# Performance work log

Measured on AMD Instinct MI355X. Metric: run time of the kernel, lower is better.

The kernel has to match this reference:

```python
import jax, jax.numpy as jnp
import numpy as np
import math

NUM_FREQS = 16  # module init num_freqs


def posenc(x, nf):
    # x [..., D] -> [..., D*2*nf]
    freqs = 2.0 ** jnp.arange(nf, dtype=x.dtype)
    xf = x[..., None] * freqs  # [..., D, nf]
    enc = jnp.concatenate([jnp.sin(xf), jnp.cos(xf)], axis=-1)  # [..., D, 2nf]
    return enc.reshape(x.shape[:-1] + (x.shape[-1] * 2 * nf,))


def plucker(rays):
    # rays [..., 6] = [origin, direction] -> [d_norm, cross(o, d_norm)]
    o, dv = rays[..., :3], rays[..., 3:]
    dn = dv / (jnp.linalg.norm(dv, axis=-1, keepdims=True) + 1e-8)
    return jnp.concatenate([dn, jnp.cross(o, dn)], axis=-1)


def grid_sample_bilinear(img, grid):
    # img [N,C,H,W], grid [N,Hg,Wg,2] in [-1,1], align_corners=True, zeros padding
    N, C, H, W = img.shape
    x = (grid[..., 0] + 1.0) * 0.5 * (W - 1)
    y = (grid[..., 1] + 1.0) * 0.5 * (H - 1)
    x0 = jnp.floor(x); x1 = x0 + 1.0
    y0 = jnp.floor(y); y1 = y0 + 1.0
    wx1 = x - x0; wx0 = 1.0 - wx1
    wy1 = y - y0; wy0 = 1.0 - wy1

    def gather(ix, iy):
        valid = ((ix >= 0) & (ix <= W - 1) & (iy >= 0) & (iy <= H - 1)).astype(img.dtype)
        ixc = jnp.clip(ix, 0, W - 1).astype(jnp.int32)
        iyc = jnp.clip(iy, 0, H - 1).astype(jnp.int32)
        vals = jax.vmap(lambda im, iyn, ixn: im[:, iyn, ixn])(img, iyc, ixc)  # [N,C,Hg,Wg]
        return vals * valid[:, None]

    return (gather(x0, y0) * (wx0 * wy0)[:, None]
            + gather(x1, y0) * (wx1 * wy0)[:, None]
            + gather(x0, y1) * (wx0 * wy1)[:, None]
            + gather(x1, y1) * (wx1 * wy1)[:, None])


def _forward(xref, mask_ref, ray_points, rays, R, T, focal, W1, b1, W2, b2, Wv, bv, Wd):
    F = NUM_FREQS
    b, n, hw, c = xref.shape
    d = ray_points.shape[3]
    res = int(math.sqrt(hw))
    # mask (already at res x res; nearest resize is identity)
    xref = xref * mask_ref.reshape(b, n, hw, 1)
    # project sample points into all n+1 camera NDC frames
    pts = ray_points[:, 0]  # [b,hw,d,3]
    p_view = jnp.einsum('bhdk,bvkj->bvhdj', pts, R) + T[:, :, None, None]  # [b,n+1,hw,d,3]
    ndc = focal[:, :, None, None, None] * p_view[..., :2] / p_view[..., 2:3]
    grid = jax.lax.stop_gradient(jnp.clip(jnp.nan_to_num(-ndc[:, 1:]), -1.2, 1.2))
    grid = grid.reshape(b * n, hw, d, 2)
    img = xref.reshape(b * n, res, res, c).transpose(0, 3, 1, 2)  # [(bn),c,res,res]
    pf = grid_sample_bilinear(img, grid)  # [(bn),c,hw,d]
    plane_features = pf.reshape(b, n, c, hw, d).transpose(0, 1, 3, 4, 2)  # [b,n,hw,d,c]

    xyz_iv = p_view                       # view-space points [b,n+1,hw,d,3]
    xyz_iv_enc = posenc(xyz_iv, F)        # [b,n+1,hw,d,6F]

    # target rays (view 0) expressed in every view frame
    o_t, d_t = rays[:, 0, :, :3], rays[:, 0, :, 3:]
    o_iv = jnp.einsum('bhk,bvkj->bvhj', o_t, R) + T[:, :, None]
    d_iv = jnp.einsum('bhk,bvkj->bvhj', d_t, R)
    cam_iv = jnp.concatenate([o_iv, d_iv], -1)[:, 1:]  # [b,n,hw,6]
    cam_iv = jnp.broadcast_to(cam_iv[:, :, :, None, :], (b, n, hw, d, 6))
    cam_iv_enc = posenc(plucker(cam_iv), F // 2)  # [b,n,hw,d,6F]

    xyz_grid = jnp.broadcast_to(xyz_iv_enc[:, :1], (b, n, hw, d, xyz_iv_enc.shape[-1]))
    # reference-view ray origins in target frame
    o_r = rays[:, 1:, :, :3]
    o_tg = jnp.einsum('bnhk,bkj->bnhj', o_r, R[:, 0]) + T[:, 0][:, None, None]
    cam_feat = jnp.broadcast_to(o_tg[:, :, :, None, :], (b, n, hw, d, 3))
    cam_feat_enc = posenc(cam_feat, F)

    plane_in = jnp.concatenate([plane_features, xyz_iv_enc[:, 1:], xyz_iv[:, 1:],
                                cam_iv_enc, cam_iv[..., 3:]], axis=-1)  # [b,n,hw,d,326]
    h = jax.nn.silu(plane_in @ W1 + b1)
    pf_final = h @ W2 + b2  # [b,n,hw,d,C]

    attn_in = jnp.concatenate([plane_features, xyz_grid,
                               jnp.broadcast_to(xyz_iv[:, :1], (b, n, hw, d, 3)),
                               cam_feat, cam_feat_enc], axis=-1)  # [b,n,hw,d,326]
    attn = jax.nn.softmax(attn_in @ Wv + bv, axis=1)  # softmax over views
    fused = (pf_final * attn).sum(1)  # [b,hw,d,C]
    out = fused @ Wd  # decoder (no bias) -> [b,hw,d,1]
    return jnp.concatenate([fused, out], axis=-1), attn


def setup_inputs() -> dict:
    B, N, RES, D, C = 1, 4, 32, 32, 128
    HW = RES * RES
    IN_DIM = C + NUM_FREQS * 3 * 4 + 6  # 326
    key = jax.random.key(0)
    ks = jax.random.split(key, 16)
    xref = jax.random.normal(ks[0], (B, N, HW, C), jnp.float32)
    mask_ref = (jax.random.uniform(ks[1], (B, N, RES, RES)) > 0.1).astype(jnp.float32)
    ray_points = jax.random.uniform(ks[2], (B, 1, HW, D, 3), minval=-0.5, maxval=0.5)
    o = jax.random.uniform(ks[3], (B, N + 1, HW, 3), minval=-0.2, maxval=0.2)
    dirs = jax.random.normal(ks[4], (B, N + 1, HW, 3))
    dirs = dirs / jnp.linalg.norm(dirs, axis=-1, keepdims=True)
    rays = jnp.concatenate([o, dirs], -1)
    R = jnp.linalg.qr(jax.random.normal(ks[5], (B, N + 1, 3, 3)))[0]
    T = jnp.concatenate([jax.random.uniform(ks[6], (B, N + 1, 2), minval=-0.2, maxval=0.2),
                         jax.random.uniform(ks[7], (B, N + 1, 1), minval=2.0, maxval=2.5)], -1)
    focal = jax.random.uniform(ks[8], (B, N + 1), minval=0.8, maxval=1.2)
    W1 = jax.random.normal(ks[9], (IN_DIM, C)) / np.sqrt(IN_DIM)
    b1 = jnp.zeros((C,), jnp.float32)
    W2 = jax.random.normal(ks[10], (C, C)) / np.sqrt(C)
    b2 = jnp.zeros((C,), jnp.float32)
    Wv = jax.random.normal(ks[11], (IN_DIM, 1)) / np.sqrt(IN_DIM)
    bv = jnp.zeros((1,), jnp.float32)
    Wd = jax.random.normal(ks[12], (C, 1)) * 0.01  # zero_module in source; small random for meaningful baseline
    return {"xref": xref, "mask_ref": mask_ref, "ray_points": ray_points, "rays": rays,
            "R": R, "T": T, "focal": focal, "W1": W1, "b1": b1, "W2": W2, "b2": b2,
            "Wv": Wv, "bv": bv, "Wd": Wd}


def reference(xref, mask_ref, ray_points, rays, R, T, focal, W1, b1, W2, b2, Wv, bv, Wd):
    return _forward(xref, mask_ref, ray_points, rays, R, T, focal, W1, b1, W2, b2, Wv, bv, Wd)
```

## Files before the change

kernel.cpp:

```cpp
#include <hip/hip_runtime.h>
#include <hip/hip_bf16.h>
#include <math.h>

#define XH 1024
#define XD 32
#define XC 128
#define XK 326

typedef __attribute__((ext_vector_type(8))) short bf16x8;
typedef __attribute__((ext_vector_type(4))) float f32x4;

__device__ __forceinline__ unsigned short f2b(float f) {
  unsigned u = __float_as_uint(f);
  return (unsigned short)((u + 0x7FFFu + ((u >> 16) & 1u)) >> 16);
}
__device__ __forceinline__ float b2f(unsigned short b) {
  return __uint_as_float(((unsigned)b) << 16);
}
__device__ __forceinline__ unsigned pk2bf(float v0, float v1) {
  __hip_bfloat162 h = __float22bfloat162_rn(make_float2(v0, v1));
  return *reinterpret_cast<unsigned*>(&h);
}

#define WT1 (12 * 8 * 64)
#define WT2 (4 * 8 * 64)

__global__ void prep_frags(const float* __restrict__ W1,
                           const float* __restrict__ W2,
                           unsigned int* __restrict__ ws) {
  int f = blockIdx.x * 256 + threadIdx.x;
  if (f >= WT1 + WT2) return;
  const float* W; int KMAX; int fl; size_t hoff, loff;
  if (f < WT1) { W = W1; KMAX = XK; fl = f; hoff = 0; loff = WT1; }
  else { W = W2; KMAX = XC; fl = f - WT1; hoff = 2 * (size_t)WT1; loff = 2 * (size_t)WT1 + WT2; }
  int l = fl & 63, ct = (fl >> 6) & 7, kc = fl >> 9;
  int c = ct * 16 + (l & 15);
  int kbase = kc * 32 + 8 * (l >> 4);
  unsigned hi[4], lo[4];
  #pragma unroll
  for (int jj = 0; jj < 4; ++jj) {
    int k0 = kbase + 2 * jj;
    float w0 = (k0     < KMAX) ? W[k0 * XC + c]       : 0.f;
    float w1 = (k0 + 1 < KMAX) ? W[(k0 + 1) * XC + c] : 0.f;
    unsigned short h0 = f2b(w0); unsigned short l0 = f2b(w0 - b2f(h0));
    unsigned short h1 = f2b(w1); unsigned short l1 = f2b(w1 - b2f(h1));
    hi[jj] = (unsigned)h0 | ((unsigned)h1 << 16);
    lo[jj] = (unsigned)l0 | ((unsigned)l1 << 16);
  }
  uint4 vh; vh.x = hi[0]; vh.y = hi[1]; vh.z = hi[2]; vh.w = hi[3];
  uint4 vl; vl.x = lo[0]; vl.y = lo[1]; vl.z = lo[2]; vl.w = lo[3];
  *(uint4*)(ws + (hoff + fl) * 4) = vh;
  *(uint4*)(ws + (loff + fl) * 4) = vl;
}


__global__ __launch_bounds__(512, 4)
void nerf_main(const float* __restrict__ xref,
               const float* __restrict__ mask,
               const float* __restrict__ rpts,
               const float* __restrict__ rays,
               const float* __restrict__ Rm,
               const float* __restrict__ Tm,
               const float* __restrict__ focp,
               const float* __restrict__ b1p,
               const float* __restrict__ b2p,
               const float* __restrict__ Wvp,
               const float* __restrict__ bvp,
               const float* __restrict__ Wdp,
               const bf16x8* __restrict__ wfrag,
               float* __restrict__ out0,
               float* __restrict__ out1)
{
  const int h = blockIdx.x;
  const int tid = threadIdx.x;

  __shared__ float sFoc[5];
  __shared__ float sRay[5][6];
  __shared__ float sOiv[5][3];
  __shared__ float sDiv[5][3];
  __shared__ float sPlk[4][6];
  __shared__ float sOtg[4][3];
  __shared__ float sPv[5][32][3];
  __shared__ float sBc[4][32][4];
  __shared__ int   sBp[4][32][4];
  __shared__ float sWv[XK];
  __shared__ float sAt[32];
  __shared__ float sBt[4];
  __shared__ float sLogit[4][32];
  __shared__ float sAw[4][32];
  __shared__ float sOutPart[4][32];
  __shared__ __align__(16) unsigned short sEnc2[4][128];
  __shared__ __align__(16) unsigned char uMem[65536];
  unsigned short* sFcHi = (unsigned short*)uMem;
  unsigned short* sFcLo = (unsigned short*)(uMem + 32768);
  unsigned short* sHbHi = (unsigned short*)(uMem + 32768);
  unsigned short* sHbLo = sHbHi + 32 * 128;
  float*          sOut  = (float*)uMem;

  for (int i = tid; i < 5;  i += 512) sFoc[i] = focp[i];
  for (int i = tid; i < 30; i += 512) { int v = i / 6, j = i % 6; sRay[v][j] = rays[(v*XH + h)*6 + j]; }
  for (int i = tid; i < XK; i += 512) sWv[i] = Wvp[i];

  if (tid < 160) {
    int v = tid >> 5, d = tid & 31;
    float p0 = rpts[(h*XD + d)*3 + 0];
    float p1 = rpts[(h*XD + d)*3 + 1];
    float p2 = rpts[(h*XD + d)*3 + 2];
    #pragma unroll
    for (int j = 0; j < 3; ++j)
      sPv[v][d][j] = p0*Rm[v*9 + j] + p1*Rm[v*9 + 3 + j] + p2*Rm[v*9 + 6 + j] + Tm[v*3 + j];
  } else if (tid < 165) {
    int v = tid - 160;
    float r0 = rays[(0*XH + h)*6 + 0], r1 = rays[(0*XH + h)*6 + 1], r2 = rays[(0*XH + h)*6 + 2];
    float r3 = rays[(0*XH + h)*6 + 3], r4 = rays[(0*XH + h)*6 + 4], r5 = rays[(0*XH + h)*6 + 5];
    #pragma unroll
    for (int j = 0; j < 3; ++j) {
      sOiv[v][j] = r0*Rm[v*9 + j] + r1*Rm[v*9 + 3 + j] + r2*Rm[v*9 + 6 + j] + Tm[v*3 + j];
      sDiv[v][j] = r3*Rm[v*9 + j] + r4*Rm[v*9 + 3 + j] + r5*Rm[v*9 + 6 + j];
    }
  }
  if (tid >= 256) {
    int t = tid - 256;
    int d = t >> 3, sub = t & 7;
    float p0 = rpts[(h*XD + d)*3 + 0];
    float p1 = rpts[(h*XD + d)*3 + 1];
    float p2 = rpts[(h*XD + d)*3 + 2];
    float pv0[3];
    #pragma unroll
    for (int j = 0; j < 3; ++j)
      pv0[j] = p0*Rm[j] + p1*Rm[3 + j] + p2*Rm[6 + j] + Tm[j];
    float p = 0.f;
    for (int kk = sub * 12; kk < sub * 12 + 12; ++kk) {
      int comp = kk >> 5, idx = kk & 31;
      float ang = pv0[comp] * (float)(1 << (idx & 15));
      float ev = (idx < 16) ? __sinf(ang) : __cosf(ang);
      p += ev * Wvp[128 + kk];
    }
    if (sub == 0)
      for (int j = 0; j < 3; ++j) p += pv0[j] * Wvp[224 + j];
    #pragma unroll
    for (int o = 1; o < 8; o <<= 1) p += __shfl_xor(p, o);
    if (sub == 0) sAt[d] = p;
  }
  __syncthreads();

  if (tid < 4) {
    int n = tid;
    float d0 = sDiv[n+1][0], d1 = sDiv[n+1][1], d2 = sDiv[n+1][2];
    float inv = 1.f / (sqrtf(d0*d0 + d1*d1 + d2*d2) + 1e-8f);
    float n0 = d0*inv, n1 = d1*inv, n2 = d2*inv;
    float o0 = sOiv[n+1][0], o1 = sOiv[n+1][1], o2 = sOiv[n+1][2];
    sPlk[n][0] = n0; sPlk[n][1] = n1; sPlk[n][2] = n2;
    sPlk[n][3] = o1*n2 - o2*n1;
    sPlk[n][4] = o2*n0 - o0*n2;
    sPlk[n][5] = o0*n1 - o1*n0;
    #pragma unroll
    for (int j = 0; j < 3; ++j)
      sOtg[n][j] = sRay[1+n][0]*Rm[j] + sRay[1+n][1]*Rm[3 + j] + sRay[1+n][2]*Rm[6 + j] + Tm[j];
  }
  if (tid >= 32 && tid < 160) {
    int idx = tid - 32, n = idx >> 5, d = idx & 31, v = n + 1;
    float px = sPv[v][d][0], py = sPv[v][d][1], pz = sPv[v][d][2], fo = sFoc[v];
    float gx = -(fo*px)/pz, gy = -(fo*py)/pz;
    if (isnan(gx)) gx = 0.f;
    if (isnan(gy)) gy = 0.f;
    gx = fminf(fmaxf(gx, -1.2f), 1.2f);
    gy = fminf(fmaxf(gy, -1.2f), 1.2f);
    float x = (gx + 1.f)*15.5f, y = (gy + 1.f)*15.5f;
    float x0f = floorf(x), y0f = floorf(y);
    float wx1 = x - x0f, wx0 = 1.f - wx1;
    float wy1 = y - y0f, wy0 = 1.f - wy1;
    int x0i = (int)x0f, y0i = (int)y0f;
    bool vx0 = (x0f >=  0.f) & (x0f <= 31.f);
    bool vx1 = (x0f >= -1.f) & (x0f <= 30.f);
    bool vy0 = (y0f >=  0.f) & (y0f <= 31.f);
    bool vy1 = (y0f >= -1.f) & (y0f <= 30.f);
    int x0c = min(max(x0i, 0), 31), x1c = min(max(x0i + 1, 0), 31);
    int y0c = min(max(y0i, 0), 31), y1c = min(max(y0i + 1, 0), 31);
    int p00 = y0c*32 + x0c, p10 = y0c*32 + x1c, p01 = y1c*32 + x0c, p11 = y1c*32 + x1c;
    sBc[n][d][0] = wx0*wy0*((vx0 && vy0) ? mask[n*XH + p00] : 0.f);
    sBc[n][d][1] = wx1*wy0*((vx1 && vy0) ? mask[n*XH + p10] : 0.f);
    sBc[n][d][2] = wx0*wy1*((vx0 && vy1) ? mask[n*XH + p01] : 0.f);
    sBc[n][d][3] = wx1*wy1*((vx1 && vy1) ? mask[n*XH + p11] : 0.f);
    sBp[n][d][0] = p00; sBp[n][d][1] = p10; sBp[n][d][2] = p01; sBp[n][d][3] = p11;
  }
  __syncthreads();

  const int brow = tid >> 2;
  const int bn = brow & 3, bd = brow >> 2;
  const int kloc0 = (tid & 3) * 16;
  float plog = 0.f;

  {
    const float* bc = sBc[bn][bd];
    const int*   bp = sBp[bn][bd];
    const float* xb = xref + bn * XH * XC;

    float4 pf[8];
    #pragma unroll
    for (int qq = 0; qq < 2; ++qq) {
      pf[qq*4+0] = *(const float4*)(xb + bp[0] * XC + kloc0 + 4 * qq);
      pf[qq*4+1] = *(const float4*)(xb + bp[1] * XC + kloc0 + 4 * qq);
      pf[qq*4+2] = *(const float4*)(xb + bp[2] * XC + kloc0 + 4 * qq);
      pf[qq*4+3] = *(const float4*)(xb + bp[3] * XC + kloc0 + 4 * qq);
    }

    {
      int n = tid >> 7, off = tid & 127;
      float val = 0.f;
      if (off >= 3 && off < 99) {
        int kk = off - 3;
        int comp = kk >> 4, idx = kk & 15;
        float ang = sPlk[n][comp] * (float)(1 << (idx & 7));
        val = (idx < 8) ? __sinf(ang) : __cosf(ang);
      } else if (off >= 99 && off < 102) {
        val = sDiv[n + 1][off - 99];
      }
      sEnc2[n][off] = f2b(val);
    }
    if (tid >= 256 && tid < 288) {
      int t = tid - 256, n = t >> 3, sub = t & 7;
      float p = 0.f;
      for (int kk = sub * 12; kk < sub * 12 + 12; ++kk) {
        int comp = kk >> 5, idx = kk & 31;
        float ang = sOtg[n][comp] * (float)(1 << (idx & 15));
        float ev = (idx < 16) ? __sinf(ang) : __cosf(ang);
        p += ev * sWv[230 + kk];
      }
      if (sub == 0) {
        for (int j = 0; j < 3; ++j) p += sOtg[n][j] * sWv[227 + j];
        p += bvp[0];
      }
      #pragma unroll
      for (int o = 1; o < 8; o <<= 1) p += __shfl_xor(p, o);
      if (sub == 0) sBt[n] = p;
    }

    {
      int kg = kloc0;
      float vv[16];
      #pragma unroll
      for (int qq = 0; qq < 4; ++qq) {
        float4 a0, a1, a2, a3;
        if (qq < 2) {
          a0 = pf[qq*4+0]; a1 = pf[qq*4+1]; a2 = pf[qq*4+2]; a3 = pf[qq*4+3];
        } else {
          a0 = *(const float4*)(xb + bp[0] * XC + kg + 4 * qq);
          a1 = *(const float4*)(xb + bp[1] * XC + kg + 4 * qq);
          a2 = *(const float4*)(xb + bp[2] * XC + kg + 4 * qq);
          a3 = *(const float4*)(xb + bp[3] * XC + kg + 4 * qq);
        }
        #pragma unroll
        for (int j = 0; j < 4; ++j)
          vv[4 * qq + j] = bc[0]*(&a0.x)[j] + bc[1]*(&a1.x)[j]
                         + bc[2]*(&a2.x)[j] + bc[3]*(&a3.x)[j];
      }
      #pragma unroll
      for (int j = 0; j < 16; ++j) plog += vv[j] * sWv[kg + j];
      #pragma unroll
      for (int qq = 0; qq < 2; ++qq) {
        unsigned ph[4], pl[4];
        #pragma unroll
        for (int j = 0; j < 4; ++j) {
          float v0 = vv[8 * qq + 2 * j], v1 = vv[8 * qq + 2 * j + 1];
          unsigned hp = pk2bf(v0, v1);
          float r0 = v0 - b2f((unsigned short)(hp & 0xFFFF));
          float r1 = v1 - b2f((unsigned short)(hp >> 16));
          ph[j] = hp;
          pl[j] = pk2bf(r0, r1);
        }
        int gidx = (brow * 128 + kg + 8 * qq) ^ ((brow & 7) << 3);
        *(uint4*)&sFcHi[gidx] = *(uint4*)ph;
        *(uint4*)&sFcLo[gidx] = *(uint4*)pl;
      }
    }
    {
      int kg = 64 + kloc0;
      float vv[16];
      #pragma unroll
      for (int qq = 0; qq < 4; ++qq) {
        float4 a0 = *(const float4*)(xb + bp[0] * XC + kg + 4 * qq);
        float4 a1 = *(const float4*)(xb + bp[1] * XC + kg + 4 * qq);
        float4 a2 = *(const float4*)(xb + bp[2] * XC + kg + 4 * qq);
        float4 a3 = *(const float4*)(xb + bp[3] * XC + kg + 4 * qq);
        #pragma unroll
        for (int j = 0; j < 4; ++j)
          vv[4 * qq + j] = bc[0]*(&a0.x)[j] + bc[1]*(&a1.x)[j]
                         + bc[2]*(&a2.x)[j] + bc[3]*(&a3.x)[j];
      }
      #pragma unroll
      for (int j = 0; j < 16; ++j) plog += vv[j] * sWv[kg + j];
      #pragma unroll
      for (int qq = 0; qq < 2; ++qq) {
        unsigned ph[4], pl[4];
        #pragma unroll
        for (int j = 0; j < 4; ++j) {
          float v0 = vv[8 * qq + 2 * j], v1 = vv[8 * qq + 2 * j + 1];
          unsigned hp = pk2bf(v0, v1);
          float r0 = v0 - b2f((unsigned short)(hp & 0xFFFF));
          float r1 = v1 - b2f((unsigned short)(hp >> 16));
          ph[j] = hp;
          pl[j] = pk2bf(r0, r1);
        }
        int gidx = (brow * 128 + kg + 8 * qq) ^ ((brow & 7) << 3);
        *(uint4*)&sFcHi[gidx] = *(uint4*)ph;
        *(uint4*)&sFcLo[gidx] = *(uint4*)pl;
      }
    }
    {
      float p = plog;
      p += __shfl_xor(p, 1);
      p += __shfl_xor(p, 2);
      if ((tid & 3) == 0) sLogit[bn][bd] = p;
    }
  }
  __syncthreads();

  if (tid < 32) {
    int d = tid;
    float l0 = sLogit[0][d] + sAt[d] + sBt[0];
    float l1 = sLogit[1][d] + sAt[d] + sBt[1];
    float l2 = sLogit[2][d] + sAt[d] + sBt[2];
    float l3 = sLogit[3][d] + sAt[d] + sBt[3];
    float m = fmaxf(fmaxf(l0, l1), fmaxf(l2, l3));
    float e0 = __expf(l0 - m), e1 = __expf(l1 - m), e2 = __expf(l2 - m), e3 = __expf(l3 - m);
    float inv = 1.f / (e0 + e1 + e2 + e3);
    float w0 = e0*inv, w1 = e1*inv, w2 = e2*inv, w3 = e3*inv;
    sAw[0][d] = w0; sAw[1][d] = w1; sAw[2][d] = w2; sAw[3][d] = w3;
    out1[(0*XH + h)*XD + d] = w0;
    out1[(1*XH + h)*XD + d] = w1;
    out1[(2*XH + h)*XD + d] = w2;
    out1[(3*XH + h)*XD + d] = w3;
  }

  const int w = tid >> 6, lane = tid & 63;
  const int rt = w & 3, cg = w >> 2;
  const int lrow = lane & 15, lg = lane >> 4;
  float bias1[4];
  #pragma unroll
  for (int ct = 0; ct < 4; ++ct) bias1[ct] = b1p[cg * 64 + ct * 16 + lrow];

  f32x4 acc1[2][4];
  #pragma unroll
  for (int rf = 0; rf < 2; ++rf)
    #pragma unroll
    for (int ct = 0; ct < 4; ++ct) acc1[rf][ct] = (f32x4){0.f, 0.f, 0.f, 0.f};

  {
    const int r0 = rt * 32 + lrow;
    const int nn = r0 & 3;
    const int dd = r0 >> 2;
    const float* pv0 = sPv[nn + 1][dd];
    const float* pv1 = sPv[nn + 1][dd + 4];
    const unsigned short* enc = sEnc2[nn];
    const float m0 = (lg & 1) ? 256.f : 1.f;
    const bool usn = (lg < 2);

    auto stepA = [&](int sk) {
      const int ai0 = (r0 * 128 + sk * 32 + 8 * lg) ^ ((r0 & 7) << 3);
      const int ai1 = ai0 + 16 * 128;
      bf16x8 ah0 = *(const bf16x8*)&sFcHi[ai0];
      bf16x8 ah1 = *(const bf16x8*)&sFcHi[ai1];
      bf16x8 al0 = *(const bf16x8*)&sFcLo[ai0];
      bf16x8 al1 = *(const bf16x8*)&sFcLo[ai1];
      const bf16x8* wkh = wfrag + (sk * 8 + cg * 4) * 64 + lane;
      const bf16x8* wkl = wkh + WT1;
      #pragma unroll
      for (int ct = 0; ct < 4; ++ct) {
        bf16x8 bh = wkh[ct * 64];
        bf16x8 bl = wkl[ct * 64];
        acc1[0][ct] = __builtin_amdgcn_mfma_f32_16x16x32_bf16(ah0, bh, acc1[0][ct], 0, 0, 0);
        acc1[0][ct] = __builtin_amdgcn_mfma_f32_16x16x32_bf16(ah0, bl, acc1[0][ct], 0, 0, 0);
        acc1[0][ct] = __builtin_amdgcn_mfma_f32_16x16x32_bf16(al0, bh, acc1[0][ct], 0, 0, 0);
        acc1[1][ct] = __builtin_amdgcn_mfma_f32_16x16x32_bf16(ah1, bh, acc1[1][ct], 0, 0, 0);
        acc1[1][ct] = __builtin_amdgcn_mfma_f32_16x16x32_bf16(ah1, bl, acc1[1][ct], 0, 0, 0);
        acc1[1][ct] = __builtin_amdgcn_mfma_f32_16x16x32_bf16(al1, bh, acc1[1][ct], 0, 0, 0);
      }
    };
    auto stepB = [&](int kc, bf16x8 A0, bf16x8 A1) {
      const bf16x8* wkh = wfrag + (kc * 8 + cg * 4) * 64 + lane;
      const bf16x8* wkl = wkh + WT1;
      #pragma unroll
      for (int ct = 0; ct < 4; ++ct) {
        bf16x8 bh = wkh[ct * 64];
        bf16x8 bl = wkl[ct * 64];
        acc1[0][ct] = __builtin_amdgcn_mfma_f32_16x16x32_bf16(A0, bh, acc1[0][ct], 0, 0, 0);
        acc1[0][ct] = __builtin_amdgcn_mfma_f32_16x16x32_bf16(A0, bl, acc1[0][ct], 0, 0, 0);
        acc1[1][ct] = __builtin_amdgcn_mfma_f32_16x16x32_bf16(A1, bh, acc1[1][ct], 0, 0, 0);
        acc1[1][ct] = __builtin_amdgcn_mfma_f32_16x16x32_bf16(A1, bl, acc1[1][ct], 0, 0, 0);
      }
    };
    auto trigf = [&](const float* pv, int comp) -> bf16x8 {
      float pA = pv[comp] * m0;
      unsigned ph[4];
      #pragma unroll
      for (int mj = 0; mj < 4; ++mj) {
        float a0f = pA * (float)(1 << (2 * mj));
        float a1f = pA * (float)(1 << (2 * mj + 1));
        float v0 = usn ? __sinf(a0f) : __cosf(a0f);
        float v1 = usn ? __sinf(a1f) : __cosf(a1f);
        ph[mj] = pk2bf(v0, v1);
      }
      union { unsigned u[4]; bf16x8 f; } cv;
      cv.u[0] = ph[0]; cv.u[1] = ph[1]; cv.u[2] = ph[2]; cv.u[3] = ph[3];
      return cv.f;
    };
    auto encf = [&](int off) -> bf16x8 {
      return *(const bf16x8*)&enc[off + lg * 8];
    };

    {
      bf16x8 t0 = trigf(pv0, 0), t1 = trigf(pv1, 0);
      stepA(0); stepB(4, t0, t1);
    }
    {
      bf16x8 t0 = trigf(pv0, 1), t1 = trigf(pv1, 1);
      stepA(1); stepB(5, t0, t1);
    }
    {
      bf16x8 t0 = trigf(pv0, 2), t1 = trigf(pv1, 2);
      stepA(2); stepB(6, t0, t1);
    }
    {
      bf16x8 e0 = encf(0);
      bf16x8 e1 = e0;
      if (lg == 0) {
        e0[0] = (short)f2b(pv0[0]); e0[1] = (short)f2b(pv0[1]); e0[2] = (short)f2b(pv0[2]);
        e1[0] = (short)f2b(pv1[0]); e1[1] = (short)f2b(pv1[1]); e1[2] = (short)f2b(pv1[2]);
      }
      stepA(3); stepB(7, e0, e1);
    }
    { bf16x8 e = encf(32); stepB(8, e, e); }
    { bf16x8 e = encf(64); stepB(9, e, e); }
    { bf16x8 e = encf(96); stepB(10, e, e); }
  }
  __syncthreads();

  #pragma unroll
  for (int rf = 0; rf < 2; ++rf) {
    int d = (rt * 2 + rf) * 4 + lg;
    float a0 = sAw[0][d], a1 = sAw[1][d], a2 = sAw[2][d], a3 = sAw[3][d];
    #pragma unroll
    for (int ct = 0; ct < 4; ++ct) {
      int c = cg * 64 + ct * 16 + lrow;
      float x0 = acc1[rf][ct][0] + bias1[ct];
      float x1 = acc1[rf][ct][1] + bias1[ct];
      float x2 = acc1[rf][ct][2] + bias1[ct];
      float x3 = acc1[rf][ct][3] + bias1[ct];
      float hb = a0 * __fdividef(x0, 1.f + __expf(-x0))
               + a1 * __fdividef(x1, 1.f + __expf(-x1))
               + a2 * __fdividef(x2, 1.f + __expf(-x2))
               + a3 * __fdividef(x3, 1.f + __expf(-x3));
      unsigned short hh = f2b(hb);
      unsigned short hl = f2b(hb - b2f(hh));
      int idx = (d * 128 + c) ^ ((d & 7) << 3);
      sHbHi[idx] = hh; sHbLo[idx] = hl;
    }
  }
  __syncthreads();

  const int rt2 = w & 1, cg2 = w >> 1;
  float bias2[2], wdv[2];
  #pragma unroll
  for (int cti = 0; cti < 2; ++cti) {
    int c = cg2 * 32 + cti * 16 + lrow;
    bias2[cti] = b2p[c]; wdv[cti] = Wdp[c];
  }
  f32x4 acc2[2];
  acc2[0] = (f32x4){0.f, 0.f, 0.f, 0.f};
  acc2[1] = (f32x4){0.f, 0.f, 0.f, 0.f};
  {
    const int ar = rt2 * 16 + lrow;
    #pragma unroll
    for (int kc = 0; kc < 4; ++kc) {
      int aidx = (ar * 128 + kc * 32 + 8 * lg) ^ ((ar & 7) << 3);
      bf16x8 ah = *(const bf16x8*)&sHbHi[aidx];
      bf16x8 al = *(const bf16x8*)&sHbLo[aidx];
      const bf16x8* wkh = wfrag + 2 * WT1 + (kc * 8 + cg2 * 2) * 64 + lane;
      const bf16x8* wkl = wkh + WT2;
      #pragma unroll
      for (int cti = 0; cti < 2; ++cti) {
        bf16x8 bh = wkh[cti * 64];
        bf16x8 bl = wkl[cti * 64];
        acc2[cti] = __builtin_amdgcn_mfma_f32_16x16x32_bf16(ah, bh, acc2[cti], 0, 0, 0);
        acc2[cti] = __builtin_amdgcn_mfma_f32_16x16x32_bf16(ah, bl, acc2[cti], 0, 0, 0);
        acc2[cti] = __builtin_amdgcn_mfma_f32_16x16x32_bf16(al, bh, acc2[cti], 0, 0, 0);
      }
    }
  }

  {
    float part[4] = {0.f, 0.f, 0.f, 0.f};
    #pragma unroll
    for (int cti = 0; cti < 2; ++cti) {
      int c = cg2 * 32 + cti * 16 + lrow;
      #pragma unroll
      for (int i = 0; i < 4; ++i) {
        int d = rt2 * 16 + lg * 4 + i;
        float fv = acc2[cti][i] + bias2[cti];
        sOut[d * 129 + c] = fv;
        part[i] += fv * wdv[cti];
      }
    }
    #pragma unroll
    for (int i = 0; i < 4; ++i) {
      float p = part[i];
      #pragma unroll
      for (int o = 1; o < 16; o <<= 1) p += __shfl_xor(p, o);
      if (lrow == 0) sOutPart[cg2][rt2 * 16 + lg * 4 + i] = p;
    }
  }
  __syncthreads();
  if (tid < 32)
    sOut[tid * 129 + 128] =
      sOutPart[0][tid] + sOutPart[1][tid] + sOutPart[2][tid] + sOutPart[3][tid];
  __syncthreads();
  {
    const float4* src = (const float4*)sOut;
    float4* dst = (float4*)(out0 + (size_t)h * (XD * 129));
    for (int i = tid; i < (XD * 129) / 4; i += 512) dst[i] = src[i];
  }
}

extern "C" void kernel_launch(void* const* d_in, const int* in_sizes, int n_in,
                              void* d_out, int out_size, void* d_ws, size_t ws_size,
                              hipStream_t stream) {
  const float* xref = (const float*)d_in[0];
  const float* mask = (const float*)d_in[1];
  const float* rpts = (const float*)d_in[2];
  const float* rays = (const float*)d_in[3];
  const float* Rm   = (const float*)d_in[4];
  const float* Tm   = (const float*)d_in[5];
  const float* foc  = (const float*)d_in[6];
  const float* W1   = (const float*)d_in[7];
  const float* b1   = (const float*)d_in[8];
  const float* W2   = (const float*)d_in[9];
  const float* b2   = (const float*)d_in[10];
  const float* Wv   = (const float*)d_in[11];
  const float* bv   = (const float*)d_in[12];
  const float* Wd   = (const float*)d_in[13];
  float* out0 = (float*)d_out;
  float* out1 = out0 + (size_t)XH * XD * 129;

  hipLaunchKernelGGL(prep_frags, dim3(32), dim3(256), 0, stream,
                     W1, W2, (unsigned int*)d_ws);
  hipLaunchKernelGGL(nerf_main, dim3(XH), dim3(512), 0, stream,
                     xref, mask, rpts, rays, Rm, Tm, foc,
                     b1, b2, Wv, bv, Wd, (const bf16x8*)d_ws, out0, out1);
}
```

Baseline: 65.51 us.

## Process two rays per block and interleave their MLP stages

Each block now handles two ray indices. Setup work for both is batched, and the first layer's MFMA for the second ray is interleaved with the epilogue and second-layer GEMM of the first ray, so trig/exp work and matrix work can overlap. Shared memory doubles to about 128KB+ and the launch bound drops to 2 blocks per CU, which lowers occupancy and raises register pressure.

```diff
diff --git a/kernel.cpp b/kernel.cpp
--- a/kernel.cpp
+++ b/kernel.cpp
@@ -54,7 +54,7 @@
 }
 
 
-__global__ __launch_bounds__(512, 4)
+__global__ __launch_bounds__(512, 2)
 void nerf_main(const float* __restrict__ xref,
                const float* __restrict__ mask,
                const float* __restrict__ rpts,
@@ -71,60 +71,66 @@
                float* __restrict__ out0,
                float* __restrict__ out1)
 {
-  const int h = blockIdx.x;
+  const int h0 = blockIdx.x * 2;
   const int tid = threadIdx.x;
 
   __shared__ float sFoc[5];
-  __shared__ float sRay[5][6];
-  __shared__ float sOiv[5][3];
-  __shared__ float sDiv[5][3];
-  __shared__ float sPlk[4][6];
-  __shared__ float sOtg[4][3];
-  __shared__ float sPv[5][32][3];
-  __shared__ float sBc[4][32][4];
-  __shared__ int   sBp[4][32][4];
+  __shared__ float sRay[2][5][6];
+  __shared__ float sOiv[2][5][3];
+  __shared__ float sDiv[2][5][3];
+  __shared__ float sPlk[2][4][6];
+  __shared__ float sOtg[2][4][3];
+  __shared__ float sPv[2][5][32][3];
+  __shared__ float sBc[2][4][32][4];
+  __shared__ int   sBp[2][4][32][4];
   __shared__ float sWv[XK];
-  __shared__ float sAt[32];
-  __shared__ float sBt[4];
-  __shared__ float sLogit[4][32];
-  __shared__ float sAw[4][32];
+  __shared__ float sAt[2][32];
+  __shared__ float sBt[2][4];
+  __shared__ float sLogit[2][4][32];
+  __shared__ float sAw[2][4][32];
   __shared__ float sOutPart[4][32];
-  __shared__ __align__(16) unsigned short sEnc2[4][128];
-  __shared__ __align__(16) unsigned char uMem[65536];
-  unsigned short* sFcHi = (unsigned short*)uMem;
-  unsigned short* sFcLo = (unsigned short*)(uMem + 32768);
-  unsigned short* sHbHi = (unsigned short*)(uMem + 32768);
-  unsigned short* sHbLo = sHbHi + 32 * 128;
-  float*          sOut  = (float*)uMem;
+  __shared__ __align__(16) unsigned short sEnc2[2][4][128];
+  __shared__ __align__(16) unsigned char uMem[131072];
+  unsigned short* sFcHi0 = (unsigned short*)uMem;
+  unsigned short* sFcLo0 = (unsigned short*)(uMem + 32768);
+  unsigned short* sHbHi0 = (unsigned short*)(uMem + 32768);
+  unsigned short* sHbLo0 = sHbHi0 + 32 * 128;
+  float*          sOut0  = (float*)uMem;
+  unsigned short* sFcHi1 = (unsigned short*)(uMem + 65536);
+  unsigned short* sFcLo1 = (unsigned short*)(uMem + 98304);
+  unsigned short* sHbHi1 = (unsigned short*)(uMem + 98304);
+  unsigned short* sHbLo1 = sHbHi1 + 32 * 128;
+  float*          sOut1  = (float*)(uMem + 65536);
 
   for (int i = tid; i < 5;  i += 512) sFoc[i] = focp[i];
-  for (int i = tid; i < 30; i += 512) { int v = i / 6, j = i % 6; sRay[v][j] = rays[(v*XH + h)*6 + j]; }
   for (int i = tid; i < XK; i += 512) sWv[i] = Wvp[i];
-
-  if (tid < 160) {
-    int v = tid >> 5, d = tid & 31;
-    float p0 = rpts[(h*XD + d)*3 + 0];
-    float p1 = rpts[(h*XD + d)*3 + 1];
-    float p2 = rpts[(h*XD + d)*3 + 2];
+  for (int i = tid; i < 60; i += 512) {
+    int hh = i / 30, r = i % 30, v = r / 6, j = r % 6;
+    sRay[hh][v][j] = rays[(v*XH + h0 + hh)*6 + j];
+  }
+  if (tid < 320) {
+    int hh = tid / 160, r = tid - hh * 160, v = r >> 5, d = r & 31, hc = h0 + hh;
+    float p0 = rpts[(hc*XD + d)*3 + 0];
+    float p1 = rpts[(hc*XD + d)*3 + 1];
+    float p2 = rpts[(hc*XD + d)*3 + 2];
     #pragma unroll
     for (int j = 0; j < 3; ++j)
-      sPv[v][d][j] = p0*Rm[v*9 + j] + p1*Rm[v*9 + 3 + j] + p2*Rm[v*9 + 6 + j] + Tm[v*3 + j];
-  } else if (tid < 165) {
-    int v = tid - 160;
-    float r0 = rays[(0*XH + h)*6 + 0], r1 = rays[(0*XH + h)*6 + 1], r2 = rays[(0*XH + h)*6 + 2];
-    float r3 = rays[(0*XH + h)*6 + 3], r4 = rays[(0*XH + h)*6 + 4], r5 = rays[(0*XH + h)*6 + 5];
+      sPv[hh][v][d][j] = p0*Rm[v*9 + j] + p1*Rm[v*9 + 3 + j] + p2*Rm[v*9 + 6 + j] + Tm[v*3 + j];
+  } else if (tid < 330) {
+    int t = tid - 320, hh = t / 5, v = t - hh * 5, hc = h0 + hh;
+    float r0 = rays[(0*XH + hc)*6 + 0], r1 = rays[(0*XH + hc)*6 + 1], r2 = rays[(0*XH + hc)*6 + 2];
+    float r3 = rays[(0*XH + hc)*6 + 3], r4 = rays[(0*XH + hc)*6 + 4], r5 = rays[(0*XH + hc)*6 + 5];
     #pragma unroll
     for (int j = 0; j < 3; ++j) {
-      sOiv[v][j] = r0*Rm[v*9 + j] + r1*Rm[v*9 + 3 + j] + r2*Rm[v*9 + 6 + j] + Tm[v*3 + j];
-      sDiv[v][j] = r3*Rm[v*9 + j] + r4*Rm[v*9 + 3 + j] + r5*Rm[v*9 + 6 + j];
-    }
-  }
-  if (tid >= 256) {
-    int t = tid - 256;
-    int d = t >> 3, sub = t & 7;
-    float p0 = rpts[(h*XD + d)*3 + 0];
-    float p1 = rpts[(h*XD + d)*3 + 1];
-    float p2 = rpts[(h*XD + d)*3 + 2];
+      sOiv[hh][v][j] = r0*Rm[v*9 + j] + r1*Rm[v*9 + 3 + j] + r2*Rm[v*9 + 6 + j] + Tm[v*3 + j];
+      sDiv[hh][v][j] = r3*Rm[v*9 + j] + r4*Rm[v*9 + 3 + j] + r5*Rm[v*9 + 6 + j];
+    }
+  }
+  {
+    int hh = tid >> 8, u = tid & 255, d = u >> 3, sub = tid & 7, hc = h0 + hh;
+    float p0 = rpts[(hc*XD + d)*3 + 0];
+    float p1 = rpts[(hc*XD + d)*3 + 1];
+    float p2 = rpts[(hc*XD + d)*3 + 2];
     float pv0[3];
     #pragma unroll
     for (int j = 0; j < 3; ++j)
@@ -140,27 +146,27 @@
       for (int j = 0; j < 3; ++j) p += pv0[j] * Wvp[224 + j];
     #pragma unroll
     for (int o = 1; o < 8; o <<= 1) p += __shfl_xor(p, o);
-    if (sub == 0) sAt[d] = p;
-  }
-  __syncthreads();
-
-  if (tid < 4) {
-    int n = tid;
-    float d0 = sDiv[n+1][0], d1 = sDiv[n+1][1], d2 = sDiv[n+1][2];
+    if (sub == 0) sAt[hh][d] = p;
+  }
+  __syncthreads();
+
+  if (tid < 8) {
+    int hh = tid >> 2, n = tid & 3;
+    float d0 = sDiv[hh][n+1][0], d1 = sDiv[hh][n+1][1], d2 = sDiv[hh][n+1][2];
     float inv = 1.f / (sqrtf(d0*d0 + d1*d1 + d2*d2) + 1e-8f);
     float n0 = d0*inv, n1 = d1*inv, n2 = d2*inv;
-    float o0 = sOiv[n+1][0], o1 = sOiv[n+1][1], o2 = sOiv[n+1][2];
-    sPlk[n][0] = n0; sPlk[n][1] = n1; sPlk[n][2] = n2;
-    sPlk[n][3] = o1*n2 - o2*n1;
-    sPlk[n][4] = o2*n0 - o0*n2;
-    sPlk[n][5] = o0*n1 - o1*n0;
+    float o0 = sOiv[hh][n+1][0], o1 = sOiv[hh][n+1][1], o2 = sOiv[hh][n+1][2];
+    sPlk[hh][n][0] = n0; sPlk[hh][n][1] = n1; sPlk[hh][n][2] = n2;
+    sPlk[hh][n][3] = o1*n2 - o2*n1;
+    sPlk[hh][n][4] = o2*n0 - o0*n2;
+    sPlk[hh][n][5] = o0*n1 - o1*n0;
     #pragma unroll
     for (int j = 0; j < 3; ++j)
-      sOtg[n][j] = sRay[1+n][0]*Rm[j] + sRay[1+n][1]*Rm[3 + j] + sRay[1+n][2]*Rm[6 + j] + Tm[j];
-  }
-  if (tid >= 32 && tid < 160) {
-    int idx = tid - 32, n = idx >> 5, d = idx & 31, v = n + 1;
-    float px = sPv[v][d][0], py = sPv[v][d][1], pz = sPv[v][d][2], fo = sFoc[v];
+      sOtg[hh][n][j] = sRay[hh][1+n][0]*Rm[j] + sRay[hh][1+n][1]*Rm[3 + j] + sRay[hh][1+n][2]*Rm[6 + j] + Tm[j];
+  }
+  if (tid >= 32 && tid < 288) {
+    int idx = tid - 32, hh = idx >> 7, r = idx & 127, n = r >> 5, d = r & 31, v = n + 1;
+    float px = sPv[hh][v][d][0], py = sPv[hh][v][d][1], pz = sPv[hh][v][d][2], fo = sFoc[v];
     float gx = -(fo*px)/pz, gy = -(fo*py)/pz;
     if (isnan(gx)) gx = 0.f;
     if (isnan(gy)) gy = 0.f;
@@ -178,23 +184,26 @@
     int x0c = min(max(x0i, 0), 31), x1c = min(max(x0i + 1, 0), 31);
     int y0c = min(max(y0i, 0), 31), y1c = min(max(y0i + 1, 0), 31);
     int p00 = y0c*32 + x0c, p10 = y0c*32 + x1c, p01 = y1c*32 + x0c, p11 = y1c*32 + x1c;
-    sBc[n][d][0] = wx0*wy0*((vx0 && vy0) ? mask[n*XH + p00] : 0.f);
-    sBc[n][d][1] = wx1*wy0*((vx1 && vy0) ? mask[n*XH + p10] : 0.f);
-    sBc[n][d][2] = wx0*wy1*((vx0 && vy1) ? mask[n*XH + p01] : 0.f);
-    sBc[n][d][3] = wx1*wy1*((vx1 && vy1) ? mask[n*XH + p11] : 0.f);
-    sBp[n][d][0] = p00; sBp[n][d][1] = p10; sBp[n][d][2] = p01; sBp[n][d][3] = p11;
+    sBc[hh][n][d][0] = wx0*wy0*((vx0 && vy0) ? mask[n*XH + p00] : 0.f);
+    sBc[hh][n][d][1] = wx1*wy0*((vx1 && vy0) ? mask[n*XH + p10] : 0.f);
+    sBc[hh][n][d][2] = wx0*wy1*((vx0 && vy1) ? mask[n*XH + p01] : 0.f);
+    sBc[hh][n][d][3] = wx1*wy1*((vx1 && vy1) ? mask[n*XH + p11] : 0.f);
+    sBp[hh][n][d][0] = p00; sBp[hh][n][d][1] = p10; sBp[hh][n][d][2] = p01; sBp[hh][n][d][3] = p11;
   }
   __syncthreads();
 
   const int brow = tid >> 2;
   const int bn = brow & 3, bd = brow >> 2;
   const int kloc0 = (tid & 3) * 16;
-  float plog = 0.f;
+  const int w = tid >> 6, lane = tid & 63;
+  const int rt = w & 3, cg = w >> 2;
+  const int lrow = lane & 15, lg = lane >> 4;
 
   {
-    const float* bc = sBc[bn][bd];
-    const int*   bp = sBp[bn][bd];
+    const float* bc = sBc[0][bn][bd];
+    const int*   bp = sBp[0][bn][bd];
     const float* xb = xref + bn * XH * XC;
+    float plog = 0.f;
 
     float4 pf[8];
     #pragma unroll
@@ -205,35 +214,35 @@
       pf[qq*4+3] = *(const float4*)(xb + bp[3] * XC + kloc0 + 4 * qq);
     }
 
-    {
-      int n = tid >> 7, off = tid & 127;
+    for (int s = tid; s < 1024; s += 512) {
+      int hh = s >> 9, n2 = (s >> 7) & 3, off = s & 127;
       float val = 0.f;
       if (off >= 3 && off < 99) {
         int kk = off - 3;
         int comp = kk >> 4, idx = kk & 15;
-        float ang = sPlk[n][comp] * (float)(1 << (idx & 7));
+        float ang = sPlk[hh][n2][comp] * (float)(1 << (idx & 7));
         val = (idx < 8) ? __sinf(ang) : __cosf(ang);
       } else if (off >= 99 && off < 102) {
-        val = sDiv[n + 1][off - 99];
-      }
-      sEnc2[n][off] = f2b(val);
-    }
-    if (tid >= 256 && tid < 288) {
-      int t = tid - 256, n = t >> 3, sub = t & 7;
+        val = sDiv[hh][n2 + 1][off - 99];
+      }
+      sEnc2[hh][n2][off] = f2b(val);
+    }
+    if (tid >= 256 && tid < 320) {
+      int t = tid - 256, hh = t >> 5, n2 = (t >> 3) & 3, sub = t & 7;
       float p = 0.f;
       for (int kk = sub * 12; kk < sub * 12 + 12; ++kk) {
         int comp = kk >> 5, idx = kk & 31;
-        float ang = sOtg[n][comp] * (float)(1 << (idx & 15));
+        float ang = sOtg[hh][n2][comp] * (float)(1 << (idx & 15));
         float ev = (idx < 16) ? __sinf(ang) : __cosf(ang);
         p += ev * sWv[230 + kk];
       }
       if (sub == 0) {
-        for (int j = 0; j < 3; ++j) p += sOtg[n][j] * sWv[227 + j];
+        for (int j = 0; j < 3; ++j) p += sOtg[hh][n2][j] * sWv[227 + j];
         p += bvp[0];
       }
       #pragma unroll
       for (int o = 1; o < 8; o <<= 1) p += __shfl_xor(p, o);
-      if (sub == 0) sBt[n] = p;
+      if (sub == 0) sBt[hh][n2] = p;
     }
 
     {
@@ -270,8 +279,8 @@
           pl[j] = pk2bf(r0, r1);
         }
         int gidx = (brow * 128 + kg + 8 * qq) ^ ((brow & 7) << 3);
-        *(uint4*)&sFcHi[gidx] = *(uint4*)ph;
-        *(uint4*)&sFcLo[gidx] = *(uint4*)pl;
+        *(uint4*)&sFcHi0[gidx] = *(uint4*)ph;
+        *(uint4*)&sFcLo0[gidx] = *(uint4*)pl;
       }
     }
     {
@@ -303,160 +312,309 @@
           pl[j] = pk2bf(r0, r1);
         }
         int gidx = (brow * 128 + kg + 8 * qq) ^ ((brow & 7) << 3);
-        *(uint4*)&sFcHi[gidx] = *(uint4*)ph;
-        *(uint4*)&sFcLo[gidx] = *(uint4*)pl;
+        *(uint4*)&sFcHi0[gidx] = *(uint4*)ph;
+        *(uint4*)&sFcLo0[gidx] = *(uint4*)pl;
       }
     }
     {
       float p = plog;
       p += __shfl_xor(p, 1);
       p += __shfl_xor(p, 2);
-      if ((tid & 3) == 0) sLogit[bn][bd] = p;
-    }
-  }
-  __syncthreads();
+      if ((tid & 3) == 0) sLogit[0][bn][bd] = p;
+    }
+  }
+  __syncthreads();
+
+  const float m0 = (lg & 1) ? 256.f : 1.f;
+  const bool usn = (lg < 2);
+  const int r0 = rt * 32 + lrow;
+  const int nn = r0 & 3;
+  const int dd = r0 >> 2;
+
+  auto trigf = [&](const float* pv, int comp) -> bf16x8 {
+    float pA = pv[comp] * m0;
+    unsigned ph[4];
+    #pragma unroll
+    for (int mj = 0; mj < 4; ++mj) {
+      float a0f = pA * (float)(1 << (2 * mj));
+      float a1f = pA * (float)(1 << (2 * mj + 1));
+      float v0 = usn ? __sinf(a0f) : __cosf(a0f);
+      float v1 = usn ? __sinf(a1f) : __cosf(a1f);
+      ph[mj] = pk2bf(v0, v1);
+    }
+    union { unsigned u[4]; bf16x8 f; } cv;
+    cv.u[0] = ph[0]; cv.u[1] = ph[1]; cv.u[2] = ph[2]; cv.u[3] = ph[3];
+    return cv.f;
+  };
+
+  float bias1[4];
+  #pragma unroll
+  for (int ct = 0; ct < 4; ++ct) bias1[ct] = b1p[cg * 64 + ct * 16 + lrow];
 
   if (tid < 32) {
     int d = tid;
-    float l0 = sLogit[0][d] + sAt[d] + sBt[0];
-    float l1 = sLogit[1][d] + sAt[d] + sBt[1];
-    float l2 = sLogit[2][d] + sAt[d] + sBt[2];
-    float l3 = sLogit[3][d] + sAt[d] + sBt[3];
+    float l0 = sLogit[0][0][d] + sAt[0][d] + sBt[0][0];
+    float l1 = sLogit[0][1][d] + sAt[0][d] + sBt[0][1];
+    float l2 = sLogit[0][2][d] + sAt[0][d] + sBt[0][2];
+    float l3 = sLogit[0][3][d] + sAt[0][d] + sBt[0][3];
     float m = fmaxf(fmaxf(l0, l1), fmaxf(l2, l3));
     float e0 = __expf(l0 - m), e1 = __expf(l1 - m), e2 = __expf(l2 - m), e3 = __expf(l3 - m);
     float inv = 1.f / (e0 + e1 + e2 + e3);
     float w0 = e0*inv, w1 = e1*inv, w2 = e2*inv, w3 = e3*inv;
-    sAw[0][d] = w0; sAw[1][d] = w1; sAw[2][d] = w2; sAw[3][d] = w3;
-    out1[(0*XH + h)*XD + d] = w0;
-    out1[(1*XH + h)*XD + d] = w1;
-    out1[(2*XH + h)*XD + d] = w2;
-    out1[(3*XH + h)*XD + d] = w3;
-  }
-
-  const int w = tid >> 6, lane = tid & 63;
-  const int rt = w & 3, cg = w >> 2;
-  const int lrow = lane & 15, lg = lane >> 4;
-  float bias1[4];
-  #pragma unroll
-  for (int ct = 0; ct < 4; ++ct) bias1[ct] = b1p[cg * 64 + ct * 16 + lrow];
-
-  f32x4 acc1[2][4];
+    sAw[0][0][d] = w0; sAw[0][1][d] = w1; sAw[0][2][d] = w2; sAw[0][3][d] = w3;
+    out1[(0*XH + h0)*XD + d] = w0;
+    out1[(1*XH + h0)*XD + d] = w1;
+    out1[(2*XH + h0)*XD + d] = w2;
+    out1[(3*XH + h0)*XD + d] = w3;
+  }
+
+  f32x4 acc1_0[2][4];
   #pragma unroll
   for (int rf = 0; rf < 2; ++rf)
     #pragma unroll
-    for (int ct = 0; ct < 4; ++ct) acc1[rf][ct] = (f32x4){0.f, 0.f, 0.f, 0.f};
+    for (int ct = 0; ct < 4; ++ct) acc1_0[rf][ct] = (f32x4){0.f, 0.f, 0.f, 0.f};
 
   {
-    const int r0 = rt * 32 + lrow;
-    const int nn = r0 & 3;
-    const int dd = r0 >> 2;
-    const float* pv0 = sPv[nn + 1][dd];
-    const float* pv1 = sPv[nn + 1][dd + 4];
-    const unsigned short* enc = sEnc2[nn];
-    const float m0 = (lg & 1) ? 256.f : 1.f;
-    const bool usn = (lg < 2);
-
-    auto stepA = [&](int sk) {
+    const float* pv00 = sPv[0][nn + 1][dd];
+    const float* pv01 = sPv[0][nn + 1][dd + 4];
+    const unsigned short* enc0 = sEnc2[0][nn];
+
+    auto stepA0 = [&](int sk) {
       const int ai0 = (r0 * 128 + sk * 32 + 8 * lg) ^ ((r0 & 7) << 3);
       const int ai1 = ai0 + 16 * 128;
-      bf16x8 ah0 = *(const bf16x8*)&sFcHi[ai0];
-      bf16x8 ah1 = *(const bf16x8*)&sFcHi[ai1];
-      bf16x8 al0 = *(const bf16x8*)&sFcLo[ai0];
-      bf16x8 al1 = *(const bf16x8*)&sFcLo[ai1];
+      bf16x8 ah0 = *(const bf16x8*)&sFcHi0[ai0];
+      bf16x8 ah1 = *(const bf16x8*)&sFcHi0[ai1];
+      bf16x8 al0 = *(const bf16x8*)&sFcLo0[ai0];
+      bf16x8 al1 = *(const bf16x8*)&sFcLo0[ai1];
       const bf16x8* wkh = wfrag + (sk * 8 + cg * 4) * 64 + lane;
       const bf16x8* wkl = wkh + WT1;
       #pragma unroll
       for (int ct = 0; ct < 4; ++ct) {
         bf16x8 bh = wkh[ct * 64];
         bf16x8 bl = wkl[ct * 64];
-        acc1[0][ct] = __builtin_amdgcn_mfma_f32_16x16x32_bf16(ah0, bh, acc1[0][ct], 0, 0, 0);
-        acc1[0][ct] = __builtin_amdgcn_mfma_f32_16x16x32_bf16(ah0, bl, acc1[0][ct], 0, 0, 0);
-        acc1[0][ct] = __builtin_amdgcn_mfma_f32_16x16x32_bf16(al0, bh, acc1[0][ct], 0, 0, 0);
-        acc1[1][ct] = __builtin_amdgcn_mfma_f32_16x16x32_bf16(ah1, bh, acc1[1][ct], 0, 0, 0);
-        acc1[1][ct] = __builtin_amdgcn_mfma_f32_16x16x32_bf16(ah1, bl, acc1[1][ct], 0, 0, 0);
-        acc1[1][ct] = __builtin_amdgcn_mfma_f32_16x16x32_bf16(al1, bh, acc1[1][ct], 0, 0, 0);
+        acc1_0[0][ct] = __builtin_amdgcn_mfma_f32_16x16x32_bf16(ah0, bh, acc1_0[0][ct], 0, 0, 0);
+        acc1_0[0][ct] = __builtin_amdgcn_mfma_f32_16x16x32_bf16(ah0, bl, acc1_0[0][ct], 0, 0, 0);
+        acc1_0[0][ct] = __builtin_amdgcn_mfma_f32_16x16x32_bf16(al0, bh, acc1_0[0][ct], 0, 0, 0);
+        acc1_0[1][ct] = __builtin_amdgcn_mfma_f32_16x16x32_bf16(ah1, bh, acc1_0[1][ct], 0, 0, 0);
+        acc1_0[1][ct] = __builtin_amdgcn_mfma_f32_16x16x32_bf16(ah1, bl, acc1_0[1][ct], 0, 0, 0);
+        acc1_0[1][ct] = __builtin_amdgcn_mfma_f32_16x16x32_bf16(al1, bh, acc1_0[1][ct], 0, 0, 0);
       }
     };
-    auto stepB = [&](int kc, bf16x8 A0, bf16x8 A1) {
+    auto stepB0 = [&](int kc, bf16x8 A0, bf16x8 A1) {
       const bf16x8* wkh = wfrag + (kc * 8 + cg * 4) * 64 + lane;
       const bf16x8* wkl = wkh + WT1;
       #pragma unroll
       for (int ct = 0; ct < 4; ++ct) {
         bf16x8 bh = wkh[ct * 64];
         bf16x8 bl = wkl[ct * 64];
-        acc1[0][ct] = __builtin_amdgcn_mfma_f32_16x16x32_bf16(A0, bh, acc1[0][ct], 0, 0, 0);
-        acc1[0][ct] = __builtin_amdgcn_mfma_f32_16x16x32_bf16(A0, bl, acc1[0][ct], 0, 0, 0);
-        acc1[1][ct] = __builtin_amdgcn_mfma_f32_16x16x32_bf16(A1, bh, acc1[1][ct], 0, 0, 0);
-        acc1[1][ct] = __builtin_amdgcn_mfma_f32_16x16x32_bf16(A1, bl, acc1[1][ct], 0, 0, 0);
+        acc1_0[0][ct] = __builtin_amdgcn_mfma_f32_16x16x32_bf16(A0, bh, acc1_0[0][ct], 0, 0, 0);
+        acc1_0[0][ct] = __builtin_amdgcn_mfma_f32_16x16x32_bf16(A0, bl, acc1_0[0][ct], 0, 0, 0);
+        acc1_0[1][ct] = __builtin_amdgcn_mfma_f32_16x16x32_bf16(A1, bh, acc1_0[1][ct], 0, 0, 0);
+        acc1_0[1][ct] = __builtin_amdgcn_mfma_f32_16x16x32_bf16(A1, bl, acc1_0[1][ct], 0, 0, 0);
       }
     };
-    auto trigf = [&](const float* pv, int comp) -> bf16x8 {
-      float pA = pv[comp] * m0;
-      unsigned ph[4];
-      #pragma unroll
-      for (int mj = 0; mj < 4; ++mj) {
-        float a0f = pA * (float)(1 << (2 * mj));
-        float a1f = pA * (float)(1 << (2 * mj + 1));
-        float v0 = usn ? __sinf(a0f) : __cosf(a0f);
-        float v1 = usn ? __sinf(a1f) : __cosf(a1f);
-        ph[mj] = pk2bf(v0, v1);
-      }
-      union { unsigned u[4]; bf16x8 f; } cv;
-      cv.u[0] = ph[0]; cv.u[1] = ph[1]; cv.u[2] = ph[2]; cv.u[3] = ph[3];
-      return cv.f;
+    auto encf0 = [&](int off) -> bf16x8 {
+      return *(const bf16x8*)&enc0[off + lg * 8];
     };
-    auto encf = [&](int off) -> bf16x8 {
-      return *(const bf16x8*)&enc[off + lg * 8];
-    };
-
+
+    const float* bc1 = sBc[1][bn][bd];
+    const int*   bp1 = sBp[1][bn][bd];
+    const float* xb  = xref + bn * XH * XC;
+    float plog1 = 0.f;
+    float4 pf[16];
+
+    #pragma unroll
+    for (int qq = 0; qq < 4; ++qq) {
+      pf[qq*4+0] = *(const float4*)(xb + bp1[0] * XC + kloc0 + 4 * qq);
+      pf[qq*4+1] = *(const float4*)(xb + bp1[1] * XC + kloc0 + 4 * qq);
+      pf[qq*4+2] = *(const float4*)(xb + bp1[2] * XC + kloc0 + 4 * qq);
+      pf[qq*4+3] = *(const float4*)(xb + bp1[3] * XC + kloc0 + 4 * qq);
+    }
+    { bf16x8 t0 = trigf(pv00, 0), t1 = trigf(pv01, 0); stepA0(0); stepB0(4, t0, t1); }
     {
-      bf16x8 t0 = trigf(pv0, 0), t1 = trigf(pv1, 0);
-      stepA(0); stepB(4, t0, t1);
-    }
+      float vv[16];
+      #pragma unroll
+      for (int qq = 0; qq < 4; ++qq)
+        #pragma unroll
+        for (int j = 0; j < 4; ++j)
+          vv[4 * qq + j] = bc1[0]*(&pf[qq*4+0].x)[j] + bc1[1]*(&pf[qq*4+1].x)[j]
+                         + bc1[2]*(&pf[qq*4+2].x)[j] + bc1[3]*(&pf[qq*4+3].x)[j];
+      #pragma unroll
+      for (int j = 0; j < 16; ++j) plog1 += vv[j] * sWv[kloc0 + j];
+      #pragma unroll
+      for (int qq = 0; qq < 2; ++qq) {
+        unsigned ph[4], pl[4];
+        #pragma unroll
+        for (int j = 0; j < 4; ++j) {
+          float v0 = vv[8 * qq + 2 * j], v1 = vv[8 * qq + 2 * j + 1];
+          unsigned hp = pk2bf(v0, v1);
+          float r0v = v0 - b2f((unsigned short)(hp & 0xFFFF));
+          float r1v = v1 - b2f((unsigned short)(hp >> 16));
+          ph[j] = hp;
+          pl[j] = pk2bf(r0v, r1v);
+        }
+        int gidx = (brow * 128 + kloc0 + 8 * qq) ^ ((brow & 7) << 3);
+        *(uint4*)&sFcHi1[gidx] = *(uint4*)ph;
+        *(uint4*)&sFcLo1[gidx] = *(uint4*)pl;
+      }
+    }
+    { bf16x8 t0 = trigf(pv00, 1), t1 = trigf(pv01, 1); stepA0(1); stepB0(5, t0, t1); }
+    #pragma unroll
+    for (int qq = 0; qq < 4; ++qq) {
+      pf[qq*4+0] = *(const float4*)(xb + bp1[0] * XC + 64 + kloc0 + 4 * qq);
+      pf[qq*4+1] = *(const float4*)(xb + bp1[1] * XC + 64 + kloc0 + 4 * qq);
+      pf[qq*4+2] = *(const float4*)(xb + bp1[2] * XC + 64 + kloc0 + 4 * qq);
+      pf[qq*4+3] = *(const float4*)(xb + bp1[3] * XC + 64 + kloc0 + 4 * qq);
+    }
+    { bf16x8 t0 = trigf(pv00, 2), t1 = trigf(pv01, 2); stepA0(2); stepB0(6, t0, t1); }
     {
-      bf16x8 t0 = trigf(pv0, 1), t1 = trigf(pv1, 1);
-      stepA(1); stepB(5, t0, t1);
+      int kg = 64 + kloc0;
+      float vv[16];
+      #pragma unroll
+      for (int qq = 0; qq < 4; ++qq)
+        #pragma unroll
+        for (int j = 0; j < 4; ++j)
+          vv[4 * qq + j] = bc1[0]*(&pf[qq*4+0].x)[j] + bc1[1]*(&pf[qq*4+1].x)[j]
+                         + bc1[2]*(&pf[qq*4+2].x)[j] + bc1[3]*(&pf[qq*4+3].x)[j];
+      #pragma unroll
+      for (int j = 0; j < 16; ++j) plog1 += vv[j] * sWv[kg + j];
+      #pragma unroll
+      for (int qq = 0; qq < 2; ++qq) {
+        unsigned ph[4], pl[4];
+        #pragma unroll
+        for (int j = 0; j < 4; ++j) {
+          float v0 = vv[8 * qq + 2 * j], v1 = vv[8 * qq + 2 * j + 1];
+          unsigned hp = pk2bf(v0, v1);
+          float r0v = v0 - b2f((unsigned short)(hp & 0xFFFF));
+          float r1v = v1 - b2f((unsigned short)(hp >> 16));
+          ph[j] = hp;
+          pl[j] = pk2bf(r0v, r1v);
+        }
+        int gidx = (brow * 128 + kg + 8 * qq) ^ ((brow & 7) << 3);
+        *(uint4*)&sFcHi1[gidx] = *(uint4*)ph;
+        *(uint4*)&sFcLo1[gidx] = *(uint4*)pl;
+      }
+      float p = plog1;
+      p += __shfl_xor(p, 1);
+      p += __shfl_xor(p, 2);
+      if ((tid & 3) == 0) sLogit[1][bn][bd] = p;
     }
     {
-      bf16x8 t0 = trigf(pv0, 2), t1 = trigf(pv1, 2);
-      stepA(2); stepB(6, t0, t1);
-    }
-    {
-      bf16x8 e0 = encf(0);
+      bf16x8 e0 = encf0(0);
       bf16x8 e1 = e0;
       if (lg == 0) {
-        e0[0] = (short)f2b(pv0[0]); e0[1] = (short)f2b(pv0[1]); e0[2] = (short)f2b(pv0[2]);
-        e1[0] = (short)f2b(pv1[0]); e1[1] = (short)f2b(pv1[1]); e1[2] = (short)f2b(pv1[2]);
-      }
-      stepA(3); stepB(7, e0, e1);
-    }
-    { bf16x8 e = encf(32); stepB(8, e, e); }
-    { bf16x8 e = encf(64); stepB(9, e, e); }
-    { bf16x8 e = encf(96); stepB(10, e, e); }
-  }
-  __syncthreads();
-
+        e0[0] = (short)f2b(pv00[0]); e0[1] = (short)f2b(pv00[1]); e0[2] = (short)f2b(pv00[2]);
+        e1[0] = (short)f2b(pv01[0]); e1[1] = (short)f2b(pv01[1]); e1[2] = (short)f2b(pv01[2]);
+      }
+      stepA0(3); stepB0(7, e0, e1);
+    }
+    { bf16x8 e = encf0(32); stepB0(8, e, e); }
+    { bf16x8 e = encf0(64); stepB0(9, e, e); }
+    { bf16x8 e = encf0(96); stepB0(10, e, e); }
+  }
+  __syncthreads();
+
+  if (tid < 32) {
+    int d = tid;
+    float l0 = sLogit[1][0][d] + sAt[1][d] + sBt[1][0];
+    float l1 = sLogit[1][1][d] + sAt[1][d] + sBt[1][1];
+    float l2 = sLogit[1][2][d] + sAt[1][d] + sBt[1][2];
+    float l3 = sLogit[1][3][d] + sAt[1][d] + sBt[1][3];
+    float m = fmaxf(fmaxf(l0, l1), fmaxf(l2, l3));
+    float e0 = __expf(l0 - m), e1 = __expf(l1 - m), e2 = __expf(l2 - m), e3 = __expf(l3 - m);
+    float inv = 1.f / (e0 + e1 + e2 + e3);
+    float w0 = e0*inv, w1 = e1*inv, w2 = e2*inv, w3 = e3*inv;
+    sAw[1][0][d] = w0; sAw[1][1][d] = w1; sAw[1][2][d] = w2; sAw[1][3][d] = w3;
+    out1[(0*XH + h0 + 1)*XD + d] = w0;
+    out1[(1*XH + h0 + 1)*XD + d] = w1;
+    out1[(2*XH + h0 + 1)*XD + d] = w2;
+    out1[(3*XH + h0 + 1)*XD + d] = w3;
+  }
+
+  f32x4 acc1_1[2][4];
   #pragma unroll
-  for (int rf = 0; rf < 2; ++rf) {
+  for (int rf = 0; rf < 2; ++rf)
+    #pragma unroll
+    for (int ct = 0; ct < 4; ++ct) acc1_1[rf][ct] = (f32x4){0.f, 0.f, 0.f, 0.f};
+
+  const float* pv10 = sPv[1][nn + 1][dd];
+  const float* pv11 = sPv[1][nn + 1][dd + 4];
+  const unsigned short* enc1 = sEnc2[1][nn];
+
+  auto stepA1 = [&](int sk) {
+    const int ai0 = (r0 * 128 + sk * 32 + 8 * lg) ^ ((r0 & 7) << 3);
+    const int ai1 = ai0 + 16 * 128;
+    bf16x8 ah0 = *(const bf16x8*)&sFcHi1[ai0];
+    bf16x8 ah1 = *(const bf16x8*)&sFcHi1[ai1];
+    bf16x8 al0 = *(const bf16x8*)&sFcLo1[ai0];
+    bf16x8 al1 = *(const bf16x8*)&sFcLo1[ai1];
+    const bf16x8* wkh = wfrag + (sk * 8 + cg * 4) * 64 + lane;
+    const bf16x8* wkl = wkh + WT1;
+    #pragma unroll
+    for (int ct = 0; ct < 4; ++ct) {
+      bf16x8 bh = wkh[ct * 64];
+      bf16x8 bl = wkl[ct * 64];
+      acc1_1[0][ct] = __builtin_amdgcn_mfma_f32_16x16x32_bf16(ah0, bh, acc1_1[0][ct], 0, 0, 0);
+      acc1_1[0][ct] = __builtin_amdgcn_mfma_f32_16x16x32_bf16(ah0, bl, acc1_1[0][ct], 0, 0, 0);
+      acc1_1[0][ct] = __builtin_amdgcn_mfma_f32_16x16x32_bf16(al0, bh, acc1_1[0][ct], 0, 0, 0);
+      acc1_1[1][ct] = __builtin_amdgcn_mfma_f32_16x16x32_bf16(ah1, bh, acc1_1[1][ct], 0, 0, 0);
+      acc1_1[1][ct] = __builtin_amdgcn_mfma_f32_16x16x32_bf16(ah1, bl, acc1_1[1][ct], 0, 0, 0);
+      acc1_1[1][ct] = __builtin_amdgcn_mfma_f32_16x16x32_bf16(al1, bh, acc1_1[1][ct], 0, 0, 0);
+    }
+  };
+  auto stepB1 = [&](int kc, bf16x8 A0, bf16x8 A1) {
+    const bf16x8* wkh = wfrag + (kc * 8 + cg * 4) * 64 + lane;
+    const bf16x8* wkl = wkh + WT1;
+    #pragma unroll
+    for (int ct = 0; ct < 4; ++ct) {
+      bf16x8 bh = wkh[ct * 64];
+      bf16x8 bl = wkl[ct * 64];
+      acc1_1[0][ct] = __builtin_amdgcn_mfma_f32_16x16x32_bf16(A0, bh, acc1_1[0][ct], 0, 0, 0);
+      acc1_1[0][ct] = __builtin_amdgcn_mfma_f32_16x16x32_bf16(A0, bl, acc1_1[0][ct], 0, 0, 0);
+      acc1_1[1][ct] = __builtin_amdgcn_mfma_f32_16x16x32_bf16(A1, bh, acc1_1[1][ct], 0, 0, 0);
+      acc1_1[1][ct] = __builtin_amdgcn_mfma_f32_16x16x32_bf16(A1, bl, acc1_1[1][ct], 0, 0, 0);
+    }
+  };
+  auto encf1 = [&](int off) -> bf16x8 {
+    return *(const bf16x8*)&enc1[off + lg * 8];
+  };
+  auto bslice0 = [&](int rf, int ct0) {
     int d = (rt * 2 + rf) * 4 + lg;
-    float a0 = sAw[0][d], a1 = sAw[1][d], a2 = sAw[2][d], a3 = sAw[3][d];
-    #pragma unroll
-    for (int ct = 0; ct < 4; ++ct) {
+    float a0 = sAw[0][0][d], a1 = sAw[0][1][d], a2 = sAw[0][2][d], a3 = sAw[0][3][d];
+    #pragma unroll
+    for (int ct = ct0; ct < ct0 + 2; ++ct) {
       int c = cg * 64 + ct * 16 + lrow;
-      float x0 = acc1[rf][ct][0] + bias1[ct];
-      float x1 = acc1[rf][ct][1] + bias1[ct];
-      float x2 = acc1[rf][ct][2] + bias1[ct];
-      float x3 = acc1[rf][ct][3] + bias1[ct];
+      float x0 = acc1_0[rf][ct][0] + bias1[ct];
+      float x1 = acc1_0[rf][ct][1] + bias1[ct];
+      float x2 = acc1_0[rf][ct][2] + bias1[ct];
+      float x3 = acc1_0[rf][ct][3] + bias1[ct];
       float hb = a0 * __fdividef(x0, 1.f + __expf(-x0))
                + a1 * __fdividef(x1, 1.f + __expf(-x1))
                + a2 * __fdividef(x2, 1.f + __expf(-x2))
                + a3 * __fdividef(x3, 1.f + __expf(-x3));
-      unsigned short hh = f2b(hb);
-      unsigned short hl = f2b(hb - b2f(hh));
+      unsigned short hhv = f2b(hb);
+      unsigned short hlv = f2b(hb - b2f(hhv));
       int idx = (d * 128 + c) ^ ((d & 7) << 3);
-      sHbHi[idx] = hh; sHbLo[idx] = hl;
-    }
-  }
+      sHbHi0[idx] = hhv; sHbLo0[idx] = hlv;
+    }
+  };
+
+  { bf16x8 t0 = trigf(pv10, 0), t1 = trigf(pv11, 0); stepA1(0); stepB1(4, t0, t1); }
+  bslice0(0, 0);
+  { bf16x8 t0 = trigf(pv10, 1), t1 = trigf(pv11, 1); stepA1(1); stepB1(5, t0, t1); }
+  bslice0(0, 2);
+  { bf16x8 t0 = trigf(pv10, 2), t1 = trigf(pv11, 2); stepA1(2); stepB1(6, t0, t1); }
+  bslice0(1, 0);
+  {
+    bf16x8 e0 = encf1(0);
+    bf16x8 e1 = e0;
+    if (lg == 0) {
+      e0[0] = (short)f2b(pv10[0]); e0[1] = (short)f2b(pv10[1]); e0[2] = (short)f2b(pv10[2]);
+      e1[0] = (short)f2b(pv11[0]); e1[1] = (short)f2b(pv11[1]); e1[2] = (short)f2b(pv11[2]);
+    }
+    stepA1(3); stepB1(7, e0, e1);
+  }
+  bslice0(1, 2);
   __syncthreads();
 
   const int rt2 = w & 1, cg2 = w >> 1;
@@ -466,30 +624,104 @@
     int c = cg2 * 32 + cti * 16 + lrow;
     bias2[cti] = b2p[c]; wdv[cti] = Wdp[c];
   }
+  const int ar = rt2 * 16 + lrow;
   f32x4 acc2[2];
   acc2[0] = (f32x4){0.f, 0.f, 0.f, 0.f};
   acc2[1] = (f32x4){0.f, 0.f, 0.f, 0.f};
+  auto g2kc0 = [&](int kc) {
+    int aidx = (ar * 128 + kc * 32 + 8 * lg) ^ ((ar & 7) << 3);
+    bf16x8 ah = *(const bf16x8*)&sHbHi0[aidx];
+    bf16x8 al = *(const bf16x8*)&sHbLo0[aidx];
+    const bf16x8* wkh = wfrag + 2 * WT1 + (kc * 8 + cg2 * 2) * 64 + lane;
+    const bf16x8* wkl = wkh + WT2;
+    #pragma unroll
+    for (int cti = 0; cti < 2; ++cti) {
+      bf16x8 bh = wkh[cti * 64];
+      bf16x8 bl = wkl[cti * 64];
+      acc2[cti] = __builtin_amdgcn_mfma_f32_16x16x32_bf16(ah, bh, acc2[cti], 0, 0, 0);
+      acc2[cti] = __builtin_amdgcn_mfma_f32_16x16x32_bf16(ah, bl, acc2[cti], 0, 0, 0);
+      acc2[cti] = __builtin_amdgcn_mfma_f32_16x16x32_bf16(al, bh, acc2[cti], 0, 0, 0);
+    }
+  };
+  { bf16x8 e = encf1(32); stepB1(8, e, e); }
+  g2kc0(0); g2kc0(1);
+  { bf16x8 e = encf1(64); stepB1(9, e, e); }
+  g2kc0(2); g2kc0(3);
+  { bf16x8 e = encf1(96); stepB1(10, e, e); }
   {
-    const int ar = rt2 * 16 + lrow;
+    float part[4] = {0.f, 0.f, 0.f, 0.f};
+    #pragma unroll
+    for (int cti = 0; cti < 2; ++cti) {
+      int c = cg2 * 32 + cti * 16 + lrow;
+      #pragma unroll
+      for (int i = 0; i < 4; ++i) {
+        int d = rt2 * 16 + lg * 4 + i;
+        float fv = acc2[cti][i] + bias2[cti];
+        sOut0[d * 129 + c] = fv;
+        part[i] += fv * wdv[cti];
+      }
+    }
+    #pragma unroll
+    for (int i = 0; i < 4; ++i) {
+      float p = part[i];
+      #pragma unroll
+      for (int o = 1; o < 16; o <<= 1) p += __shfl_xor(p, o);
+      if (lrow == 0) sOutPart[cg2][rt2 * 16 + lg * 4 + i] = p;
+    }
+  }
+  __syncthreads();
+
+  if (tid < 32)
+    sOut0[tid * 129 + 128] =
+      sOutPart[0][tid] + sOutPart[1][tid] + sOutPart[2][tid] + sOutPart[3][tid];
+  #pragma unroll
+  for (int rf = 0; rf < 2; ++rf) {
+    int d = (rt * 2 + rf) * 4 + lg;
+    float a0 = sAw[1][0][d], a1 = sAw[1][1][d], a2 = sAw[1][2][d], a3 = sAw[1][3][d];
+    #pragma unroll
+    for (int ct = 0; ct < 4; ++ct) {
+      int c = cg * 64 + ct * 16 + lrow;
+      float x0 = acc1_1[rf][ct][0] + bias1[ct];
+      float x1 = acc1_1[rf][ct][1] + bias1[ct];
+      float x2 = acc1_1[rf][ct][2] + bias1[ct];
+      float x3 = acc1_1[rf][ct][3] + bias1[ct];
+      float hb = a0 * __fdividef(x0, 1.f + __expf(-x0))
+               + a1 * __fdividef(x1, 1.f + __expf(-x1))
+               + a2 * __fdividef(x2, 1.f + __expf(-x2))
+               + a3 * __fdividef(x3, 1.f + __expf(-x3));
+      unsigned short hhv = f2b(hb);
+      unsigned short hlv = f2b(hb - b2f(hhv));
+      int idx = (d * 128 + c) ^ ((d & 7) << 3);
+      sHbHi1[idx] = hhv; sHbLo1[idx] = hlv;
+    }
+  }
+  __syncthreads();
+
+  {
+    const float4* src = (const float4*)sOut0;
+    float4* dst = (float4*)(out0 + (size_t)h0 * (XD * 129));
+    for (int i = tid; i < (XD * 129) / 4; i += 512) dst[i] = src[i];
+  }
+  {
+    f32x4 acc2b[2];
+    acc2b[0] = (f32x4){0.f, 0.f, 0.f, 0.f};
+    acc2b[1] = (f32x4){0.f, 0.f, 0.f, 0.f};
     #pragma unroll
     for (int kc = 0; kc < 4; ++kc) {
       int aidx = (ar * 128 + kc * 32 + 8 * lg) ^ ((ar & 7) << 3);
-      bf16x8 ah = *(const bf16x8*)&sHbHi[aidx];
-      bf16x8 al = *(const bf16x8*)&sHbLo[aidx];
+      bf16x8 ah = *(const bf16x8*)&sHbHi1[aidx];
+      bf16x8 al = *(const bf16x8*)&sHbLo1[aidx];
       const bf16x8* wkh = wfrag + 2 * WT1 + (kc * 8 + cg2 * 2) * 64 + lane;
       const bf16x8* wkl = wkh + WT2;
       #pragma unroll
       for (int cti = 0; cti < 2; ++cti) {
         bf16x8 bh = wkh[cti * 64];
         bf16x8 bl = wkl[cti * 64];
-        acc2[cti] = __builtin_amdgcn_mfma_f32_16x16x32_bf16(ah, bh, acc2[cti], 0, 0, 0);
-        acc2[cti] = __builtin_amdgcn_mfma_f32_16x16x32_bf16(ah, bl, acc2[cti], 0, 0, 0);
-        acc2[cti] = __builtin_amdgcn_mfma_f32_16x16x32_bf16(al, bh, acc2[cti], 0, 0, 0);
-      }
-    }
-  }
-
-  {
+        acc2b[cti] = __builtin_amdgcn_mfma_f32_16x16x32_bf16(ah, bh, acc2b[cti], 0, 0, 0);
+        acc2b[cti] = __builtin_amdgcn_mfma_f32_16x16x32_bf16(ah, bl, acc2b[cti], 0, 0, 0);
+        acc2b[cti] = __builtin_amdgcn_mfma_f32_16x16x32_bf16(al, bh, acc2b[cti], 0, 0, 0);
+      }
+    }
     float part[4] = {0.f, 0.f, 0.f, 0.f};
     #pragma unroll
     for (int cti = 0; cti < 2; ++cti) {
@@ -497,8 +729,8 @@
       #pragma unroll
       for (int i = 0; i < 4; ++i) {
         int d = rt2 * 16 + lg * 4 + i;
-        float fv = acc2[cti][i] + bias2[cti];
-        sOut[d * 129 + c] = fv;
+        float fv = acc2b[cti][i] + bias2[cti];
+        sOut1[d * 129 + c] = fv;
         part[i] += fv * wdv[cti];
       }
     }
@@ -511,13 +743,14 @@
     }
   }
   __syncthreads();
+
   if (tid < 32)
-    sOut[tid * 129 + 128] =
+    sOut1[tid * 129 + 128] =
       sOutPart[0][tid] + sOutPart[1][tid] + sOutPart[2][tid] + sOutPart[3][tid];
   __syncthreads();
   {
-    const float4* src = (const float4*)sOut;
-    float4* dst = (float4*)(out0 + (size_t)h * (XD * 129));
+    const float4* src = (const float4*)sOut1;
+    float4* dst = (float4*)(out0 + (size_t)(h0 + 1) * (XD * 129));
     for (int i = tid; i < (XD * 129) / 4; i += 512) dst[i] = src[i];
   }
 }
@@ -544,7 +777,7 @@
 
   hipLaunchKernelGGL(prep_frags, dim3(32), dim3(256), 0, stream,
                      W1, W2, (unsigned int*)d_ws);
-  hipLaunchKernelGGL(nerf_main, dim3(XH), dim3(512), 0, stream,
+  hipLaunchKernelGGL(nerf_main, dim3(XH / 2), dim3(512), 0, stream,
                      xref, mask, rpts, rays, Rm, Tm, foc,
                      b1, b2, Wv, bv, Wd, (const bf16x8*)d_ws, out0, out1);
 }
```

Result: slower. 74.37 us (+13.5%).
